# Kernel optimization log

Hardware: AMD Instinct MI355X
Metric: run time of the kernel (lower is better)

The kernel has to match this reference:

```python
import jax, jax.numpy as jnp
import numpy as np

NUM_HEADS = 16


def setup_inputs() -> dict:
    key = jax.random.key(0)
    ks = jax.random.split(key, 6)
    B, S, H = 4, 2048, 1024
    x = jax.random.normal(ks[0], (B, S, H), dtype=jnp.float32)
    mask = jax.random.randint(ks[1], (B, 1, 1, S), 0, 2, dtype=jnp.int32)
    scale = 1.0 / np.sqrt(H)
    Wq = jax.random.normal(ks[2], (H, H), dtype=jnp.float32) * scale
    Wk = jax.random.normal(ks[3], (H, H), dtype=jnp.float32) * scale
    Wv = jax.random.normal(ks[4], (H, H), dtype=jnp.float32) * scale
    Wo = jax.random.normal(ks[5], (H, H), dtype=jnp.float32) * scale
    bo = jnp.zeros((H,), dtype=jnp.float32)
    return {"x": x, "mask": mask, "Wq": Wq, "Wk": Wk, "Wv": Wv, "Wo": Wo, "bo": bo}


def reference(x, mask, Wq, Wk, Wv, Wo, bo):
    B, S, H = x.shape
    nh = NUM_HEADS
    dk = H // nh

    def split_heads(t):  # (B,S,H) -> (B,nh,S,dk)
        return t.reshape(B, S, nh, dk).transpose(0, 2, 1, 3)

    # torch Linear: y = x @ W.T (q/k/v bias-free)
    q = split_heads(x @ Wq.T)
    k = split_heads(x @ Wk.T)
    v = split_heads(x @ Wv.T)

    scores = jnp.einsum('bhqd,bhkd->bhqk', q, k) / jnp.sqrt(jnp.float32(dk))
    scores = jnp.where(mask == 0, jnp.float32(-1e9), scores)
    attn = jax.nn.softmax(scores, axis=-1)  # dropout is identity in eval mode
    out = jnp.einsum('bhqk,bhkd->bhqd', attn, v)
    out = out.transpose(0, 2, 1, 3).reshape(B, S, H)
    return out @ Wo.T + bo
```

## Files before the change

### kernel.cpp

```cpp
#include <hip/hip_runtime.h>
#include <hip/hip_bf16.h>

typedef __attribute__((ext_vector_type(8))) short sh8;
typedef __attribute__((ext_vector_type(4))) float f32x4;

#define MFMA16(a, b, c) __builtin_amdgcn_mfma_f32_16x16x32_bf16((a), (b), (c), 0, 0, 0)

__device__ __forceinline__ unsigned short f2bf(float f) {
    return (unsigned short)((__float_as_uint(f) + 0x8000u) >> 16);
}
__device__ __forceinline__ unsigned int pack2bf(float lo, float hi) {
    unsigned int ul = __float_as_uint(lo) + 0x8000u;
    unsigned int uh = __float_as_uint(hi) + 0x8000u;
    return __builtin_amdgcn_perm(uh, ul, 0x07060302u);
}
__device__ __forceinline__ float redmax_hi(float x) {
    x = fmaxf(x, __shfl_xor(x, 16, 64));
    return fmaxf(x, __shfl_xor(x, 32, 64));
}
__device__ __forceinline__ float redsum_hi(float x) {
    x += __shfl_xor(x, 16, 64);
    return x + __shfl_xor(x, 32, 64);
}
__device__ __forceinline__ void gload_lds16(const void* g, void* l) {
    __builtin_amdgcn_global_load_lds(
        (const __attribute__((address_space(1))) unsigned int*)g,
        (__attribute__((address_space(3))) unsigned int*)l, 16, 0, 0);
}

__global__ __launch_bounds__(256) void cvt_x_k(
    const float* __restrict__ src, unsigned short* __restrict__ dst, int n4)
{
    int i = blockIdx.x * 256 + threadIdx.x;
    int stride = gridDim.x * 256;
    for (; i < n4; i += stride) {
        float4 v = ((const float4*)src)[i];
        uint2 h = { pack2bf(v.x, v.y), pack2bf(v.z, v.w) };
        ((uint2*)dst)[i] = h;
    }
}
__global__ __launch_bounds__(256) void cvt_w_k(
    const float* __restrict__ Wq, const float* __restrict__ Wk,
    const float* __restrict__ Wv, const float* __restrict__ Wo,
    unsigned short* __restrict__ wbf)
{
    int i = blockIdx.x * 256 + threadIdx.x;
    int seg = i >> 18;
    int off = i & 0x3FFFF;
    const float* s = (seg < 2) ? ((seg == 0) ? Wq : Wk) : ((seg == 2) ? Wv : Wo);
    float4 v = ((const float4*)s)[off];
    uint2 h = { pack2bf(v.x, v.y), pack2bf(v.z, v.w) };
    ((uint2*)wbf)[i] = h;
}

__global__ __launch_bounds__(64) void compact_k(
    const int* __restrict__ mask, int* __restrict__ idx, int* __restrict__ cnt)
{
    const int b = blockIdx.x, l = threadIdx.x;
    const int* mb = mask + b * 2048;
    int base = 0;
    for (int i = 0; i < 32; ++i) {
        int m = mb[i * 64 + l];
        unsigned long long bal = __ballot(m != 0);
        int pre = __popcll(bal & ((1ull << l) - 1ull));
        if (m) idx[b * 2048 + base + pre] = i * 64 + l;
        base += (int)__popcll(bal);
    }
    if (base == 0) {
        for (int i = l; i < 2048; i += 64) idx[b * 2048 + i] = i;
        base = 2048;
    }
    if (l == 0) cnt[b] = base;
}

__global__ __launch_bounds__(256) void kvgather_k(
    const unsigned short* __restrict__ qkv, const int* __restrict__ idx,
    const int* __restrict__ cnt, unsigned short* __restrict__ Kck, int b0)
{
    const int b = blockIdx.z;
    const int t = blockIdx.y;
    const int z = blockIdx.x;
    const int nc = cnt[b0 + b];
    if (t * 64 >= ((nc + 63) & ~63)) return;
    const int* idxb = idx + (size_t)(b0 + b) * 2048;
    const int tid = threadIdx.x;
    unsigned short* dst_b = Kck + (size_t)b * 2048 * 1024;
#pragma unroll
    for (int p = 0; p < 4; ++p) {
        int i = p * 256 + tid;
        int r = t * 64 + z * 8 + (i >> 7);
        int c = i & 127;
        int src = idxb[min(r, nc - 1)];
        uint4 v = *(const uint4*)&qkv[((size_t)b * 2048 + src) * 3072 + 1024 + c * 8];
        *(uint4*)&dst_b[(size_t)r * 1024 + c * 8] = v;
    }
}

__global__ __launch_bounds__(256) void vtrans_k(
    const unsigned short* __restrict__ qkv, const int* __restrict__ idx,
    const int* __restrict__ cnt, unsigned short* __restrict__ Vtg, int b0)
{
    __shared__ unsigned short Ls[128][72];
    const int kb = blockIdx.x;
    const int h  = blockIdx.y;
    const int b  = blockIdx.z;
    const int nc = cnt[b0 + b];
    if (kb * 128 >= ((nc + 63) & ~63)) return;
    const int* idxb = idx + (size_t)(b0 + b) * 2048;
    const int tid = threadIdx.x;
#pragma unroll
    for (int p = 0; p < 4; ++p) {
        int i = p * 256 + tid;
        int r = i >> 3, c = i & 7;
        int src = idxb[min(kb * 128 + r, nc - 1)];
        uint4 v = *(const uint4*)&qkv[((size_t)b * 2048 + src) * 3072 + 2048 + h * 64 + c * 8];
        *(uint4*)&Ls[r][c * 8] = v;
    }
    __syncthreads();
    unsigned short* dst = Vtg + ((size_t)b * 16 + h) * 64 * 2048;
#pragma unroll
    for (int p = 0; p < 4; ++p) {
        int i = p * 256 + tid;
        int d = i >> 4, kc = i & 15;
        unsigned int wv[4];
#pragma unroll
        for (int j = 0; j < 4; ++j) {
            unsigned int lo = Ls[kc * 8 + 2 * j][d];
            unsigned int hv = Ls[kc * 8 + 2 * j + 1][d];
            wv[j] = lo | (hv << 16);
        }
        *(uint4*)&dst[(size_t)d * 2048 + kb * 128 + kc * 8] = *(uint4*)wv;
    }
}

__global__ __launch_bounds__(256) void gemm_qkv_k(
    const unsigned short* __restrict__ xbf,
    const unsigned short* __restrict__ wbf,
    unsigned short* __restrict__ qkv)
{
    __shared__ unsigned short As[128][32];
    __shared__ unsigned short Bs[128][32];
    const int tid = threadIdx.x;
    const int l = tid & 63, w = tid >> 6;
    const int wr = w >> 1, wc = w & 1;
    const long row0 = (long)blockIdx.y * 128;
    const int col0 = blockIdx.x * 128;

    f32x4 acc[4][4] = {};
    const int fr = l & 15, hi = l >> 4;

    const int sr = tid >> 2;
    const int sc = (tid & 3) * 8;
    const unsigned short* ga = &xbf[(row0 + sr) * 1024 + sc];
    const unsigned short* gb = &wbf[(long)(col0 + sr) * 1024 + sc];
    unsigned short* la = &As[w * 16][0];
    unsigned short* lb = &Bs[w * 16][0];

    for (int k0 = 0; k0 < 1024; k0 += 32) {
        __syncthreads();
        gload_lds16(ga + k0, la);
        gload_lds16(ga + 64 * 1024 + k0, la + 64 * 32);
        gload_lds16(gb + k0, lb);
        gload_lds16(gb + 64 * 1024 + k0, lb + 64 * 32);
        __syncthreads();

        sh8 af[4], bf[4];
#pragma unroll
        for (int i = 0; i < 4; ++i) {
            af[i] = *(const sh8*)&As[wr * 64 + i * 16 + fr][hi * 8];
            bf[i] = *(const sh8*)&Bs[wc * 64 + i * 16 + fr][hi * 8];
        }
#pragma unroll
        for (int i = 0; i < 4; ++i)
#pragma unroll
            for (int j = 0; j < 4; ++j)
                acc[i][j] = MFMA16(af[i], bf[j], acc[i][j]);
    }

    const float scale = (col0 < 1024) ? 0.1803368801f : 1.0f;
    const int rg = hi * 4, cg = l & 15;
#pragma unroll
    for (int i = 0; i < 4; ++i)
#pragma unroll
        for (int j = 0; j < 4; ++j) {
            long gr = row0 + wr * 64 + i * 16 + rg;
            int gc = col0 + wc * 64 + j * 16 + cg;
#pragma unroll
            for (int r = 0; r < 4; ++r)
                qkv[(gr + r) * 3072 + gc] = f2bf(acc[i][j][r] * scale);
        }
}

__global__ __launch_bounds__(256) void attn_k(
    const unsigned short* __restrict__ qkv, const unsigned short* __restrict__ Kck,
    const unsigned short* __restrict__ Vtg, const int* __restrict__ cnt,
    unsigned short* __restrict__ ao, int b0)
{
    __shared__ unsigned short Kl[64][64];
    __shared__ unsigned short Vt[64][64];
    __shared__ float biasf[64];
    __shared__ unsigned short Pl[4][16][72];

    const int tid = threadIdx.x;
    const int l = tid & 63, w = tid >> 6;
    const int fr = l & 15, hi = l >> 4;

    int nwg = gridDim.x;
    int wgid = ((nwg & 7) == 0) ? ((blockIdx.x & 7) * (nwg >> 3) + (blockIdx.x >> 3))
                                : blockIdx.x;
    const int qb = wgid & 31;
    const int h  = (wgid >> 5) & 15;
    const int b  = wgid >> 9;
    const int q0 = qb * 64;
    const long base = (long)b * 2048;

    const int nc = cnt[b0 + b];
    const int nt = (nc + 63) >> 6;

    sh8 qf0, qf1;
    {
        const unsigned short* qp = &qkv[(base + q0 + w * 16 + fr) * 3072 + h * 64 + hi * 8];
        qf0 = *(const sh8*)qp;
        qf1 = *(const sh8*)(qp + 32);
    }

    f32x4 acc[4] = {};
    float mrow = -1e30f;
    float lrow = 0.f;

    const long TSK = 131072;
    const char* kck_b = (const char*)Kck + (size_t)b * 2048 * 2048;

    const int l8 = l >> 3, c8 = l & 7;
    const char* ksrc = kck_b + (size_t)(w * 16 + l8) * 2048 + h * 128 + ((c8 ^ l8) * 16);
    unsigned short* kdst0 = &Kl[w * 16][0];
    unsigned short* kdst1 = &Kl[w * 16 + 8][0];

    const char* vtg_h = (const char*)Vtg + ((size_t)b * 16 + h) * 64 * 4096;
    const int d0 = w * 16 + l8, d1 = d0 + 8;
    const int fd0 = (d0 & 7) ^ (d0 >> 3), fd1 = (d1 & 7) ^ (d1 >> 3);
    const char* vsrc0 = vtg_h + (size_t)d0 * 4096 + ((c8 ^ fd0) * 16);
    const char* vsrc1 = vtg_h + (size_t)d1 * 4096 + ((c8 ^ fd1) * 16);
    unsigned short* vdst0 = &Vt[w * 16][0];
    unsigned short* vdst1 = &Vt[w * 16 + 8][0];

    if (tid < 64) biasf[tid] = ((nt - 1) * 64 + tid < nc) ? 0.0f : -1e9f;

    for (int t = 0; t < nt; ++t) {
        __syncthreads();
        gload_lds16(ksrc, kdst0);
        gload_lds16(ksrc + 8 * 2048, kdst1);
        ksrc += TSK;
        gload_lds16(vsrc0, vdst0);
        gload_lds16(vsrc1, vdst1);
        vsrc0 += 128; vsrc1 += 128;
        __syncthreads();

        sh8 kf[4][2];
#pragma unroll
        for (int tt = 0; tt < 4; ++tt) {
            const unsigned short* kp = &Kl[tt * 16 + fr][0];
#pragma unroll
            for (int c = 0; c < 2; ++c)
                kf[tt][c] = *(const sh8*)&kp[((4 * c + hi) ^ (fr & 7)) * 8];
        }

        f32x4 s[4] = {};
        __builtin_amdgcn_s_setprio(1);
#pragma unroll
        for (int tt = 0; tt < 4; ++tt) {
            s[tt] = MFMA16(kf[tt][0], qf0, s[tt]);
            s[tt] = MFMA16(kf[tt][1], qf1, s[tt]);
        }
        __builtin_amdgcn_s_setprio(0);

        if (t == nt - 1) {
#pragma unroll
            for (int tt = 0; tt < 4; ++tt)
                s[tt] += *(const f32x4*)&biasf[tt * 16 + 4 * hi];
        }

        float pm = s[0][0];
#pragma unroll
        for (int tt = 0; tt < 4; ++tt)
#pragma unroll
            for (int r = 0; r < 4; ++r) pm = fmaxf(pm, s[tt][r]);
        pm = redmax_hi(pm);

        if (!__all(pm <= mrow)) {
            float mn = fmaxf(mrow, pm);
            float scl = __builtin_amdgcn_exp2f(mrow - mn);
            lrow *= scl;
#pragma unroll
            for (int df = 0; df < 4; ++df) acc[df] *= scl;
            mrow = mn;
        }

        float ps = 0.f;
#pragma unroll
        for (int tt = 0; tt < 4; ++tt)
#pragma unroll
            for (int r = 0; r < 4; ++r) {
                float p = __builtin_amdgcn_exp2f(s[tt][r] - mrow);
                s[tt][r] = p;
                ps += p;
            }
        lrow += redsum_hi(ps);

#pragma unroll
        for (int tt = 0; tt < 4; ++tt) {
            uint2 pw = { pack2bf(s[tt][0], s[tt][1]), pack2bf(s[tt][2], s[tt][3]) };
            *(uint2*)&Pl[w][fr][tt * 16 + hi * 4] = pw;
        }

#pragma unroll
        for (int c = 0; c < 2; ++c) {
            sh8 pa = *(const sh8*)&Pl[w][fr][c * 32 + hi * 8];
            __builtin_amdgcn_s_setprio(1);
#pragma unroll
            for (int df = 0; df < 4; ++df) {
                int d = df * 16 + fr;
                int fd = (d & 7) ^ (d >> 3);
                sh8 vfr = *(const sh8*)&Vt[d][((4 * c + hi) ^ fd) * 8];
                acc[df] = MFMA16(vfr, pa, acc[df]);
            }
            __builtin_amdgcn_s_setprio(0);
        }
    }

    {
        float inv = 1.0f / lrow;
        long qr = base + q0 + w * 16 + fr;
        unsigned short* op = &ao[qr * 1024 + h * 64];
#pragma unroll
        for (int df = 0; df < 4; ++df) {
            f32x4 o = acc[df];
            uint2 ow = { pack2bf(o[0] * inv, o[1] * inv), pack2bf(o[2] * inv, o[3] * inv) };
            *(uint2*)&op[df * 16 + hi * 4] = ow;
        }
    }
}

__global__ __launch_bounds__(256) void gemm_out_k(
    const unsigned short* __restrict__ ao, const unsigned short* __restrict__ wob,
    const float* __restrict__ bo, float* __restrict__ out)
{
    __shared__ unsigned short As[128][32];
    __shared__ unsigned short Bs[128][32];
    const int tid = threadIdx.x;
    const int l = tid & 63, w = tid >> 6;
    const int wr = w >> 1, wc = w & 1;
    const long row0 = (long)blockIdx.y * 128;
    const int col0 = blockIdx.x * 128;

    f32x4 acc[4][4] = {};
    const int fr = l & 15, hi = l >> 4;

    const int sr = tid >> 2;
    const int sc = (tid & 3) * 8;
    const unsigned short* ga = &ao[(row0 + sr) * 1024 + sc];
    const unsigned short* gb = &wob[(long)(col0 + sr) * 1024 + sc];
    unsigned short* la = &As[w * 16][0];
    unsigned short* lb = &Bs[w * 16][0];

    for (int k0 = 0; k0 < 1024; k0 += 32) {
        __syncthreads();
        gload_lds16(ga + k0, la);
        gload_lds16(ga + 64 * 1024 + k0, la + 64 * 32);
        gload_lds16(gb + k0, lb);
        gload_lds16(gb + 64 * 1024 + k0, lb + 64 * 32);
        __syncthreads();

        sh8 af[4], bf[4];
#pragma unroll
        for (int i = 0; i < 4; ++i) {
            af[i] = *(const sh8*)&As[wr * 64 + i * 16 + fr][hi * 8];
            bf[i] = *(const sh8*)&Bs[wc * 64 + i * 16 + fr][hi * 8];
        }
#pragma unroll
        for (int i = 0; i < 4; ++i)
#pragma unroll
            for (int j = 0; j < 4; ++j)
                acc[i][j] = MFMA16(af[i], bf[j], acc[i][j]);
    }

    const int rg = hi * 4, cg = l & 15;
#pragma unroll
    for (int i = 0; i < 4; ++i)
#pragma unroll
        for (int j = 0; j < 4; ++j) {
            long gr = row0 + wr * 64 + i * 16 + rg;
            int gc = col0 + wc * 64 + j * 16 + cg;
            float bb = bo[gc];
#pragma unroll
            for (int r = 0; r < 4; ++r)
                out[(gr + r) * 1024 + gc] = acc[i][j][r] + bb;
        }
}

extern "C" void kernel_launch(void* const* d_in, const int* in_sizes, int n_in,
                              void* d_out, int out_size, void* d_ws, size_t ws_size,
                              hipStream_t stream) {
    const float* x    = (const float*)d_in[0];
    const int*   mask = (const int*)d_in[1];
    const float* Wq   = (const float*)d_in[2];
    const float* Wk   = (const float*)d_in[3];
    const float* Wv   = (const float*)d_in[4];
    const float* Wo   = (const float*)d_in[5];
    const float* bo   = (const float*)d_in[6];
    float* out = (float*)d_out;

    const size_t wbf_bytes = (size_t)4096 * 1024 * 2;
    const size_t idx_bytes = (size_t)4 * 2048 * 4 + 64;
    const size_t xbf_per_b = (size_t)2048 * 1024 * 2;
    const size_t qkv_per_b = (size_t)2048 * 3072 * 2;
    const size_t ao_per_b  = (size_t)2048 * 1024 * 2;
    const size_t kck_per_b = (size_t)2048 * 1024 * 2;
    const size_t vt_per_b  = (size_t)16 * 64 * 2048 * 2;
    const size_t per_b = xbf_per_b + qkv_per_b + ao_per_b + kck_per_b + vt_per_b;

    size_t fixed = wbf_bytes + idx_bytes;
    size_t avail = (ws_size > fixed) ? (ws_size - fixed) : 0;
    int bchunk = (avail >= per_b) ? (int)(avail / per_b) : 1;
    if (bchunk > 4) bchunk = 4;

    char* p = (char*)d_ws;
    unsigned short* wbf = (unsigned short*)p;            p += wbf_bytes;
    int* idxp = (int*)p;                                 p += (size_t)4 * 2048 * 4;
    int* cntp = (int*)p;                                 p += 64;
    unsigned short* xbf = (unsigned short*)p;            p += (size_t)bchunk * xbf_per_b;
    unsigned short* qkv = (unsigned short*)p;            p += (size_t)bchunk * qkv_per_b;
    unsigned short* ao  = (unsigned short*)p;            p += (size_t)bchunk * ao_per_b;
    unsigned short* Kck = (unsigned short*)p;            p += (size_t)bchunk * kck_per_b;
    unsigned short* Vtg = (unsigned short*)p;

    cvt_w_k<<<4096, 256, 0, stream>>>(Wq, Wk, Wv, Wo, wbf);
    compact_k<<<4, 64, 0, stream>>>(mask, idxp, cntp);

    for (int b0 = 0; b0 < 4; b0 += bchunk) {
        int bc = (4 - b0 < bchunk) ? (4 - b0) : bchunk;
        cvt_x_k<<<2048, 256, 0, stream>>>(
            x + (size_t)b0 * 2048 * 1024, xbf, bc * 524288);
        gemm_qkv_k<<<dim3(24, bc * 16), 256, 0, stream>>>(xbf, wbf, qkv);
        kvgather_k<<<dim3(8, 32, bc), 256, 0, stream>>>(qkv, idxp, cntp, Kck, b0);
        vtrans_k<<<dim3(16, 16, bc), 256, 0, stream>>>(qkv, idxp, cntp, Vtg, b0);
        attn_k<<<dim3(512 * bc), 256, 0, stream>>>(qkv, Kck, Vtg, cntp, ao, b0);
        gemm_out_k<<<dim3(8, bc * 16), 256, 0, stream>>>(
            ao, wbf + (size_t)3072 * 1024, bo, out + (size_t)b0 * 2048 * 1024);
    }
}
```

Measured before the change: 213.5 us.

## Gather unmasked x rows before projection and write K/V-transposed directly from GEMM

Compacts the unmasked rows of x before the projection instead of gathering K and V afterwards. K and V are then projected only for the surviving key rows, roughly halving the K/V GEMM work with a random mask. The GEMM epilogue writes K compacted and V already transposed, which removes the separate kvgather and vtrans kernels. The cost is an extra x-gather pass and strided 8-byte V stores in the epilogue.

```diff
diff --git a/kernel.cpp b/kernel.cpp
--- a/kernel.cpp
+++ b/kernel.cpp
@@ -73,9 +73,9 @@
     if (l == 0) cnt[b] = base;
 }
 
-__global__ __launch_bounds__(256) void kvgather_k(
-    const unsigned short* __restrict__ qkv, const int* __restrict__ idx,
-    const int* __restrict__ cnt, unsigned short* __restrict__ Kck, int b0)
+__global__ __launch_bounds__(256) void xgather_k(
+    const unsigned short* __restrict__ xbf, const int* __restrict__ idx,
+    const int* __restrict__ cnt, unsigned short* __restrict__ xc, int b0)
 {
     const int b = blockIdx.z;
     const int t = blockIdx.y;
@@ -84,75 +84,48 @@
     if (t * 64 >= ((nc + 63) & ~63)) return;
     const int* idxb = idx + (size_t)(b0 + b) * 2048;
     const int tid = threadIdx.x;
-    unsigned short* dst_b = Kck + (size_t)b * 2048 * 1024;
 #pragma unroll
     for (int p = 0; p < 4; ++p) {
         int i = p * 256 + tid;
         int r = t * 64 + z * 8 + (i >> 7);
         int c = i & 127;
         int src = idxb[min(r, nc - 1)];
-        uint4 v = *(const uint4*)&qkv[((size_t)b * 2048 + src) * 3072 + 1024 + c * 8];
-        *(uint4*)&dst_b[(size_t)r * 1024 + c * 8] = v;
-    }
-}
-
-__global__ __launch_bounds__(256) void vtrans_k(
-    const unsigned short* __restrict__ qkv, const int* __restrict__ idx,
-    const int* __restrict__ cnt, unsigned short* __restrict__ Vtg, int b0)
-{
-    __shared__ unsigned short Ls[128][72];
-    const int kb = blockIdx.x;
-    const int h  = blockIdx.y;
-    const int b  = blockIdx.z;
-    const int nc = cnt[b0 + b];
-    if (kb * 128 >= ((nc + 63) & ~63)) return;
-    const int* idxb = idx + (size_t)(b0 + b) * 2048;
-    const int tid = threadIdx.x;
-#pragma unroll
-    for (int p = 0; p < 4; ++p) {
-        int i = p * 256 + tid;
-        int r = i >> 3, c = i & 7;
-        int src = idxb[min(kb * 128 + r, nc - 1)];
-        uint4 v = *(const uint4*)&qkv[((size_t)b * 2048 + src) * 3072 + 2048 + h * 64 + c * 8];
-        *(uint4*)&Ls[r][c * 8] = v;
-    }
-    __syncthreads();
-    unsigned short* dst = Vtg + ((size_t)b * 16 + h) * 64 * 2048;
-#pragma unroll
-    for (int p = 0; p < 4; ++p) {
-        int i = p * 256 + tid;
-        int d = i >> 4, kc = i & 15;
-        unsigned int wv[4];
-#pragma unroll
-        for (int j = 0; j < 4; ++j) {
-            unsigned int lo = Ls[kc * 8 + 2 * j][d];
-            unsigned int hv = Ls[kc * 8 + 2 * j + 1][d];
-            wv[j] = lo | (hv << 16);
-        }
-        *(uint4*)&dst[(size_t)d * 2048 + kb * 128 + kc * 8] = *(uint4*)wv;
-    }
-}
-
-__global__ __launch_bounds__(256) void gemm_qkv_k(
-    const unsigned short* __restrict__ xbf,
-    const unsigned short* __restrict__ wbf,
-    unsigned short* __restrict__ qkv)
+        uint4 v = *(const uint4*)&xbf[((size_t)b * 2048 + src) * 1024 + c * 8];
+        *(uint4*)&xc[((size_t)b * 2048 + r) * 1024 + c * 8] = v;
+    }
+}
+
+__global__ __launch_bounds__(256) void gemm_proj_k(
+    const unsigned short* __restrict__ xbf, const unsigned short* __restrict__ xc,
+    const unsigned short* __restrict__ wbf, const int* __restrict__ cnt, int b0,
+    unsigned short* __restrict__ qb, unsigned short* __restrict__ Kck,
+    unsigned short* __restrict__ Vtg)
 {
     __shared__ unsigned short As[128][32];
     __shared__ unsigned short Bs[128][32];
     const int tid = threadIdx.x;
     const int l = tid & 63, w = tid >> 6;
     const int wr = w >> 1, wc = w & 1;
-    const long row0 = (long)blockIdx.y * 128;
-    const int col0 = blockIdx.x * 128;
+    const int bx = blockIdx.x;
+    const int bl = blockIdx.y >> 4;
+    const int rl = (blockIdx.y & 15) * 128;
+    const int mode = (bx < 8) ? 0 : ((bx < 16) ? 1 : 2);
+
+    if (mode != 0) {
+        int ncp = (cnt[b0 + bl] + 63) & ~63;
+        if (rl >= ncp) return;
+    }
+    const long row0 = (long)bl * 2048 + rl;
+    const unsigned short* Asrc = (mode == 0) ? xbf : xc;
+    const int wrow0 = (mode == 0) ? bx * 128 : (1024 + (bx - 8) * 128);
 
     f32x4 acc[4][4] = {};
     const int fr = l & 15, hi = l >> 4;
 
     const int sr = tid >> 2;
     const int sc = (tid & 3) * 8;
-    const unsigned short* ga = &xbf[(row0 + sr) * 1024 + sc];
-    const unsigned short* gb = &wbf[(long)(col0 + sr) * 1024 + sc];
+    const unsigned short* ga = &Asrc[(row0 + sr) * 1024 + sc];
+    const unsigned short* gb = &wbf[(long)(wrow0 + sr) * 1024 + sc];
     unsigned short* la = &As[w * 16][0];
     unsigned short* lb = &Bs[w * 16][0];
 
@@ -177,22 +150,39 @@
                 acc[i][j] = MFMA16(af[i], bf[j], acc[i][j]);
     }
 
-    const float scale = (col0 < 1024) ? 0.1803368801f : 1.0f;
     const int rg = hi * 4, cg = l & 15;
-#pragma unroll
-    for (int i = 0; i < 4; ++i)
-#pragma unroll
-        for (int j = 0; j < 4; ++j) {
-            long gr = row0 + wr * 64 + i * 16 + rg;
-            int gc = col0 + wc * 64 + j * 16 + cg;
-#pragma unroll
-            for (int r = 0; r < 4; ++r)
-                qkv[(gr + r) * 3072 + gc] = f2bf(acc[i][j][r] * scale);
-        }
+    if (mode == 2) {
+#pragma unroll
+        for (int i = 0; i < 4; ++i)
+#pragma unroll
+            for (int j = 0; j < 4; ++j) {
+                int feat = (bx - 8) * 128 + wc * 64 + j * 16 + cg - 1024;
+                int hh = feat >> 6, dd = feat & 63;
+                long kv = rl + wr * 64 + i * 16 + rg;
+                unsigned short* vt = Vtg + ((size_t)(bl * 16 + hh) * 64 + dd) * 2048 + kv;
+                uint2 ow = { pack2bf(acc[i][j][0], acc[i][j][1]),
+                             pack2bf(acc[i][j][2], acc[i][j][3]) };
+                *(uint2*)vt = ow;
+            }
+    } else {
+        unsigned short* outp = (mode == 0) ? qb : Kck;
+        const float scale = (mode == 0) ? 0.1803368801f : 1.0f;
+        const int c0 = (mode == 0) ? bx * 128 : (bx - 8) * 128;
+#pragma unroll
+        for (int i = 0; i < 4; ++i)
+#pragma unroll
+            for (int j = 0; j < 4; ++j) {
+                long gr = row0 + wr * 64 + i * 16 + rg;
+                int gc = c0 + wc * 64 + j * 16 + cg;
+#pragma unroll
+                for (int r = 0; r < 4; ++r)
+                    outp[(gr + r) * 1024 + gc] = f2bf(acc[i][j][r] * scale);
+            }
+    }
 }
 
 __global__ __launch_bounds__(256) void attn_k(
-    const unsigned short* __restrict__ qkv, const unsigned short* __restrict__ Kck,
+    const unsigned short* __restrict__ qb, const unsigned short* __restrict__ Kck,
     const unsigned short* __restrict__ Vtg, const int* __restrict__ cnt,
     unsigned short* __restrict__ ao, int b0)
 {
@@ -208,10 +198,10 @@
     int nwg = gridDim.x;
     int wgid = ((nwg & 7) == 0) ? ((blockIdx.x & 7) * (nwg >> 3) + (blockIdx.x >> 3))
                                 : blockIdx.x;
-    const int qb = wgid & 31;
+    const int qb_ = wgid & 31;
     const int h  = (wgid >> 5) & 15;
     const int b  = wgid >> 9;
-    const int q0 = qb * 64;
+    const int q0 = qb_ * 64;
     const long base = (long)b * 2048;
 
     const int nc = cnt[b0 + b];
@@ -219,7 +209,7 @@
 
     sh8 qf0, qf1;
     {
-        const unsigned short* qp = &qkv[(base + q0 + w * 16 + fr) * 3072 + h * 64 + hi * 8];
+        const unsigned short* qp = &qb[(base + q0 + w * 16 + fr) * 1024 + h * 64 + hi * 8];
         qf0 = *(const sh8*)qp;
         qf1 = *(const sh8*)(qp + 32);
     }
@@ -412,12 +402,8 @@
 
     const size_t wbf_bytes = (size_t)4096 * 1024 * 2;
     const size_t idx_bytes = (size_t)4 * 2048 * 4 + 64;
-    const size_t xbf_per_b = (size_t)2048 * 1024 * 2;
-    const size_t qkv_per_b = (size_t)2048 * 3072 * 2;
-    const size_t ao_per_b  = (size_t)2048 * 1024 * 2;
-    const size_t kck_per_b = (size_t)2048 * 1024 * 2;
-    const size_t vt_per_b  = (size_t)16 * 64 * 2048 * 2;
-    const size_t per_b = xbf_per_b + qkv_per_b + ao_per_b + kck_per_b + vt_per_b;
+    const size_t seg_b = (size_t)2048 * 1024 * 2;
+    const size_t per_b = 6 * seg_b;
 
     size_t fixed = wbf_bytes + idx_bytes;
     size_t avail = (ws_size > fixed) ? (ws_size - fixed) : 0;
@@ -428,11 +414,12 @@
     unsigned short* wbf = (unsigned short*)p;            p += wbf_bytes;
     int* idxp = (int*)p;                                 p += (size_t)4 * 2048 * 4;
     int* cntp = (int*)p;                                 p += 64;
-    unsigned short* xbf = (unsigned short*)p;            p += (size_t)bchunk * xbf_per_b;
-    unsigned short* qkv = (unsigned short*)p;            p += (size_t)bchunk * qkv_per_b;
-    unsigned short* ao  = (unsigned short*)p;            p += (size_t)bchunk * ao_per_b;
-    unsigned short* Kck = (unsigned short*)p;            p += (size_t)bchunk * kck_per_b;
-    unsigned short* Vtg = (unsigned short*)p;
+    unsigned short* xbf = (unsigned short*)p;            p += (size_t)bchunk * seg_b;
+    unsigned short* xc  = (unsigned short*)p;            p += (size_t)bchunk * seg_b;
+    unsigned short* qbp = (unsigned short*)p;            p += (size_t)bchunk * seg_b;
+    unsigned short* Kck = (unsigned short*)p;            p += (size_t)bchunk * seg_b;
+    unsigned short* Vtg = (unsigned short*)p;            p += (size_t)bchunk * seg_b;
+    unsigned short* ao  = (unsigned short*)p;
 
     cvt_w_k<<<4096, 256, 0, stream>>>(Wq, Wk, Wv, Wo, wbf);
     compact_k<<<4, 64, 0, stream>>>(mask, idxp, cntp);
@@ -441,10 +428,10 @@
         int bc = (4 - b0 < bchunk) ? (4 - b0) : bchunk;
         cvt_x_k<<<2048, 256, 0, stream>>>(
             x + (size_t)b0 * 2048 * 1024, xbf, bc * 524288);
-        gemm_qkv_k<<<dim3(24, bc * 16), 256, 0, stream>>>(xbf, wbf, qkv);
-        kvgather_k<<<dim3(8, 32, bc), 256, 0, stream>>>(qkv, idxp, cntp, Kck, b0);
-        vtrans_k<<<dim3(16, 16, bc), 256, 0, stream>>>(qkv, idxp, cntp, Vtg, b0);
-        attn_k<<<dim3(512 * bc), 256, 0, stream>>>(qkv, Kck, Vtg, cntp, ao, b0);
+        xgather_k<<<dim3(8, 32, bc), 256, 0, stream>>>(xbf, idxp, cntp, xc, b0);
+        gemm_proj_k<<<dim3(24, 16 * bc), 256, 0, stream>>>(
+            xbf, xc, wbf, cntp, b0, qbp, Kck, Vtg);
+        attn_k<<<dim3(512 * bc), 256, 0, stream>>>(qbp, Kck, Vtg, cntp, ao, b0);
         gemm_out_k<<<dim3(8, bc * 16), 256, 0, stream>>>(
             ao, wbf + (size_t)3072 * 1024, bo, out + (size_t)b0 * 2048 * 1024);
     }
```

Measured after the change: 211.9 us. Within noise of the previous version (-0.8%).
